# Kernel optimization log

Measured on AMD Instinct MI355X. Metric: run time of the kernel, lower is better.

## Reference

```python
import jax, jax.numpy as jnp
import numpy as np

N_BLOCKS, N_LAYERS = 3, 10
DILATIONS = [2 ** l for _ in range(N_BLOCKS) for l in range(N_LAYERS)] + [1]


def dilate(x, new, old):
    """nsynth-style batch-folding dilation: [n,c,l] -> [n*new/old, c, l*old/new]."""
    if new == old:
        return x
    n, c, l = x.shape
    n_new = n * new // old
    l_new = l * old // new
    # (n,c,l) -> (c,l,n) -> (c,l_new,n_new) -> (n_new,c,l_new)
    return jnp.transpose(jnp.transpose(x, (1, 2, 0)).reshape(c, l_new, n_new), (2, 0, 1))


def conv1d(x, w, b=None, pad=0):
    y = jax.lax.conv_general_dilated(
        x, w, window_strides=(1,), padding=[(pad, pad)],
        dimension_numbers=("NCH", "OIH", "NCH"))
    if b is not None:
        y = y + b[None, :, None]
    return y


def setup_inputs() -> dict:
    key = jax.random.key(0)
    ks = jax.random.split(key, 13)
    s = 0.05
    R, S, Cin, Cout, K, L = 256, 256, 1, 256, 3, 4096
    nl = N_BLOCKS * N_LAYERS
    return {
        "x": jax.random.normal(ks[0], (2, Cin, L), jnp.float32),
        "init_w": jax.random.normal(ks[1], (R, Cin, K), jnp.float32) * s,
        "init_b": jax.random.normal(ks[2], (R,), jnp.float32) * s,
        "iskip_w": jax.random.normal(ks[3], (S, R, 1), jnp.float32) * s,
        "iskip_b": jax.random.normal(ks[4], (S,), jnp.float32) * s,
        "gate_w": jax.random.normal(ks[5], (nl, R, R, K), jnp.float32) * s,
        "gate_b": jax.random.normal(ks[6], (nl, R), jnp.float32) * s,
        "feat_w": jax.random.normal(ks[7], (nl, R, R, K), jnp.float32) * s,
        "feat_b": jax.random.normal(ks[8], (nl, R), jnp.float32) * s,
        "skip_w": jax.random.normal(ks[9], (nl, S, R, 1), jnp.float32) * s,
        "thru_w": jax.random.normal(ks[10], (nl, R, R, 1), jnp.float32) * s,
        "final_w": jax.random.normal(ks[11], (Cout, S, 1), jnp.float32) * s,
        "final_b": jax.random.normal(ks[12], (Cout,), jnp.float32) * s,
    }


def reference(x, init_w, init_b, iskip_w, iskip_b, gate_w, gate_b,
              feat_w, feat_b, skip_w, thru_w, final_w, final_b):
    pad = (init_w.shape[-1] - 1) // 2  # kernel_size=3 -> pad=1
    h = conv1d(x, init_w, init_b, pad=pad)          # [n, R, L]
    s = conv1d(h, iskip_w, iskip_b)                 # [n, S, L]
    for k in range(N_BLOCKS * N_LAYERS):
        d_new, d_old = DILATIONS[k], DILATIONS[k - 1]
        hd = dilate(h, d_new, d_old)                # [n*d, R, L/d]
        g = conv1d(hd, gate_w[k], gate_b[k], pad=pad)
        f = conv1d(hd, feat_w[k], feat_b[k], pad=pad)
        res = jax.nn.sigmoid(g) * jnp.tanh(f)
        h = hd + conv1d(res, thru_w[k])
        s = s + dilate(conv1d(res, skip_w[k]), 1, d_new)
    return conv1d(s, final_w, final_b)
```

## Files before the change

kernel.cpp:

```cpp
#include <hip/hip_runtime.h>


#define TS 8192
#define NL 30
#define NBLK 256

typedef __attribute__((ext_vector_type(8))) short bf16x8;
typedef __attribute__((ext_vector_type(4))) float f32x4;

__device__ __forceinline__ unsigned short f2bf(float f) {
    union { float f; unsigned int u; } v; v.f = f;
    unsigned int u = v.u;
    u += 0x7fffu + ((u >> 16) & 1u);
    return (unsigned short)(u >> 16);
}

__device__ __forceinline__ void gload_lds16(const void* g, void* l) {
    __builtin_amdgcn_global_load_lds(
        (const __attribute__((address_space(1))) void*)g,
        (__attribute__((address_space(3))) void*)l, 16, 0, 0);
}

#define VMW8()  asm volatile("s_waitcnt vmcnt(8)" ::: "memory")
#define VMW4()  asm volatile("s_waitcnt vmcnt(4)" ::: "memory")
#define VMW0()  asm volatile("s_waitcnt vmcnt(0)" ::: "memory")
#define LGKM0() asm volatile("s_waitcnt lgkmcnt(0)" ::: "memory")
#define SBAR()  __builtin_amdgcn_s_barrier()
#define MFMA16(a, b, c) __builtin_amdgcn_mfma_f32_16x16x32_bf16((a), (b), (c), 0, 0, 0)

__device__ __forceinline__ int swz_jb(int bid) {
    return ((bid & 7) << 5) | (bid >> 3);
}

__global__ void prep_weights_kernel(
    const float* __restrict__ gw, const float* __restrict__ fw,
    const float* __restrict__ tw, const float* __restrict__ sw,
    const float* __restrict__ iw, const float* __restrict__ fnw,
    unsigned short* __restrict__ Wgf, unsigned short* __restrict__ Wts,
    unsigned short* __restrict__ Wib, unsigned short* __restrict__ Wfb)
{
    const int idx = blockIdx.x * blockDim.x + threadIdx.x;
    const int stride = gridDim.x * blockDim.x;
    const int n_gf = NL * 3 * 512 * 256;
    for (int i = idx; i < n_gf; i += stride) {
        int ci = i & 255;
        int o  = (i >> 8) & 511;
        int r  = i >> 17;
        int t  = r % 3;
        int k  = r / 3;
        float v = (o < 256) ? gw[((k * 256 + o) * 256 + ci) * 3 + t]
                            : fw[((k * 256 + (o - 256)) * 256 + ci) * 3 + t];
        Wgf[i] = f2bf(v);
    }
    const int n_ts = NL * 512 * 256;
    for (int i = idx; i < n_ts; i += stride) {
        int ci = i & 255;
        int o  = (i >> 8) & 511;
        int k  = i >> 17;
        float v = (o < 256) ? tw[(k * 256 + o) * 256 + ci]
                            : sw[(k * 256 + (o - 256)) * 256 + ci];
        Wts[i] = f2bf(v);
    }
    for (int i = idx; i < 256 * 256; i += stride) Wib[i] = f2bf(iw[i]);
    for (int i = idx; i < 256 * 256; i += stride) Wfb[i] = f2bf(fnw[i]);
}

__device__ __forceinline__ void grid_barrier(unsigned* cnt, unsigned target, int tid) {
    __syncthreads();
    if (tid == 0) {
        __hip_atomic_fetch_add(cnt, 1u, __ATOMIC_RELEASE, __HIP_MEMORY_SCOPE_AGENT);
        while (__hip_atomic_load(cnt, __ATOMIC_RELAXED, __HIP_MEMORY_SCOPE_AGENT) < target)
            __builtin_amdgcn_s_sleep(2);
        (void)__hip_atomic_load(cnt, __ATOMIC_ACQUIRE, __HIP_MEMORY_SCOPE_AGENT);
    }
    __syncthreads();
}

__device__ __forceinline__ void stage_chunk(
    const unsigned short* __restrict__ Wgf_k,
    const unsigned short* __restrict__ Wts_k,
    unsigned short* B_lds, int c, int w, int lane)
{
    const int buf  = c % 3;
    const int rsub = lane >> 2;
    const int slot = (lane & 3) ^ ((lane >> 3) & 3);
    unsigned short* dst = B_lds + w * 6144 + buf * 2048;
    if (c < 24) {
        const int t = c >> 3, kc = c & 7;
        const unsigned short* Wb = Wgf_k + (t * 512 + 32 * w) * 256 + kc * 32 + slot * 8;
        #pragma unroll
        for (int q = 0; q < 4; ++q) {
            const int r_loc = q * 16 + rsub;
            const int grow  = (q < 2) ? r_loc : (224 + r_loc);
            gload_lds16(Wb + grow * 256, dst + q * 512);
        }
    } else {
        const int kc = c - 24;
        const unsigned short* Wb = Wts_k + (64 * w) * 256 + kc * 32 + slot * 8;
        #pragma unroll
        for (int q = 0; q < 4; ++q)
            gload_lds16(Wb + (q * 16 + rsub) * 256, dst + q * 512);
    }
}

__device__ __forceinline__ bf16x8 bread(const unsigned short* Bw, int r, int krow)
{
    const int slot = krow ^ ((r >> 1) & 3);
    return *(const bf16x8*)(Bw + r * 32 + slot * 8);
}

__global__ __launch_bounds__(512, 2)
void wavenet_kernel(const float* __restrict__ x,
                    const float* __restrict__ init_w,
                    const float* __restrict__ init_b,
                    const unsigned short* __restrict__ Wib,
                    const float* __restrict__ ib,
                    const unsigned short* __restrict__ Wgf,
                    const unsigned short* __restrict__ Wts,
                    const float* __restrict__ gbA,
                    const float* __restrict__ fbA,
                    const unsigned short* __restrict__ Wfb,
                    const float* __restrict__ fbias,
                    unsigned short* __restrict__ Hb0,
                    unsigned short* __restrict__ Hb1,
                    float* __restrict__ out,
                    unsigned* __restrict__ counter)
{
    __shared__ __align__(16) unsigned short A_lds[3 * 32 * 256];
    __shared__ __align__(16) unsigned short B_lds[8 * 3 * 2048];

    const int tid  = threadIdx.x;
    const int lane = tid & 63;
    const int w    = tid >> 6;
    const int j0   = swz_jb(blockIdx.x) * 32;
    const int arow = lane & 15;
    const int krow = lane >> 4;
    const int aswz = (arow & 7) << 4;
    const int cg0  = w * 32;
    const int c0   = w * 64;
    const int cs0  = (w - 4) * 64;

    f32x4 state[2][4];

    if (w < 4) {
        #pragma unroll
        for (int rt = 0; rt < 2; ++rt)
            #pragma unroll
            for (int fc = 0; fc < 4; ++fc) {
                #pragma unroll
                for (int i = 0; i < 4; ++i) {
                    const int row = rt * 16 + krow * 4 + i;
                    const int col = c0 + fc * 16 + arow;
                    const int j   = j0 + row;
                    float acc = init_b[col];
                    #pragma unroll
                    for (int t = 0; t < 3; ++t) {
                        const int i2 = j + 2 * t - 2;
                        if (i2 >= 0 && i2 < TS)
                            acc += init_w[col * 3 + t] * x[(i2 & 1) * 4096 + (i2 >> 1)];
                    }
                    state[rt][fc][i] = acc;
                    const unsigned short hb = f2bf(acc);
                    Hb0[(j << 8) + col] = hb;
                    A_lds[((32 + row) << 8) + (((col << 1) ^ ((row & 7) << 4)) >> 1)] = hb;
                }
            }
    }
    LGKM0(); SBAR();

    if (w >= 4) {
        #pragma unroll
        for (int rt = 0; rt < 2; ++rt)
            #pragma unroll
            for (int fc = 0; fc < 4; ++fc) {
                const float b = ib[cs0 + fc * 16 + arow];
                state[rt][fc] = (f32x4){b, b, b, b};
            }
        #pragma unroll
        for (int kc = 0; kc < 8; ++kc) {
            const int aoff = ((kc * 64 + krow * 16) ^ aswz) >> 1;
            const bf16x8 a0 = *(const bf16x8*)(A_lds + ((32 + arow) << 8) + aoff);
            const bf16x8 a1 = *(const bf16x8*)(A_lds + ((48 + arow) << 8) + aoff);
            const int koff = kc * 32 + krow * 8;
            #pragma unroll
            for (int fc = 0; fc < 4; ++fc) {
                const bf16x8 bb = *(const bf16x8*)(Wib + ((cs0 + fc * 16 + arow) << 8) + koff);
                state[0][fc] = MFMA16(a0, bb, state[0][fc]);
                state[1][fc] = MFMA16(a1, bb, state[1][fc]);
            }
        }
    }

    stage_chunk(Wgf, Wts, B_lds, 0, w, lane);
    stage_chunk(Wgf, Wts, B_lds, 1, w, lane);

    unsigned target = NBLK;
    grid_barrier(counter, target, tid);

    const unsigned short* Hb_in = Hb0;
    unsigned short*       Hb_out = Hb1;

    for (int k = 0; k < NL; ++k) {
        const int d = 2 << (k % 10);
        const unsigned short* Wgf_k = Wgf + (size_t)k * 3 * 512 * 256;
        const unsigned short* Wts_k = Wts + (size_t)k * 512 * 256;
        const float gv0 = gbA[k * 256 + cg0 + arow];
        const float gv1 = gbA[k * 256 + cg0 + 16 + arow];
        const float fv0 = fbA[k * 256 + cg0 + arow];
        const float fv1 = fbA[k * 256 + cg0 + 16 + arow];

        #pragma unroll
        for (int q = 0; q < 4; ++q) {
            const int cc  = tid + q * 512;
            const int c16 = cc & 31;
            const int m   = (cc >> 5) & 31;
            const int t   = (cc >> 10) << 1;
            const int r   = j0 + m + (t - 1) * d;
            uint4 v = make_uint4(0u, 0u, 0u, 0u);
            if (r >= 0 && r < TS)
                v = *(const uint4*)(Hb_in + (r << 8) + (c16 << 3));
            const int sb = (c16 << 4) ^ ((m & 7) << 4);
            *(uint4*)(A_lds + ((t * 32 + m) << 8) + (sb >> 1)) = v;
        }
        LGKM0(); SBAR();

        f32x4 accG[2][2], accF[2][2];
        accG[0][0] = (f32x4){gv0, gv0, gv0, gv0};
        accG[1][0] = accG[0][0];
        accG[0][1] = (f32x4){gv1, gv1, gv1, gv1};
        accG[1][1] = accG[0][1];
        accF[0][0] = (f32x4){fv0, fv0, fv0, fv0};
        accF[1][0] = accF[0][0];
        accF[0][1] = (f32x4){fv1, fv1, fv1, fv1};
        accF[1][1] = accF[0][1];

        #pragma unroll
        for (int c = 0; c < 24; ++c) {
            stage_chunk(Wgf_k, Wts_k, B_lds, c + 2, w, lane);
            VMW8();
            const int t = c >> 3, kc = c & 7;
            const int aoff = ((kc * 64 + krow * 16) ^ aswz) >> 1;
            const unsigned short* At = A_lds + ((t * 32 + arow) << 8);
            const bf16x8 a0 = *(const bf16x8*)(At + aoff);
            const bf16x8 a1 = *(const bf16x8*)(At + (16 << 8) + aoff);
            const unsigned short* Bw = B_lds + w * 6144 + (c % 3) * 2048;
            const bf16x8 bg0 = bread(Bw, arow, krow);
            const bf16x8 bg1 = bread(Bw, 16 + arow, krow);
            const bf16x8 bf0 = bread(Bw, 32 + arow, krow);
            const bf16x8 bf1 = bread(Bw, 48 + arow, krow);
            accG[0][0] = MFMA16(a0, bg0, accG[0][0]);
            accG[1][0] = MFMA16(a1, bg0, accG[1][0]);
            accG[0][1] = MFMA16(a0, bg1, accG[0][1]);
            accG[1][1] = MFMA16(a1, bg1, accG[1][1]);
            accF[0][0] = MFMA16(a0, bf0, accF[0][0]);
            accF[1][0] = MFMA16(a1, bf0, accF[1][0]);
            accF[0][1] = MFMA16(a0, bf1, accF[0][1]);
            accF[1][1] = MFMA16(a1, bf1, accF[1][1]);
        }

        LGKM0(); SBAR();

        #pragma unroll
        for (int rt = 0; rt < 2; ++rt)
            #pragma unroll
            for (int fc = 0; fc < 2; ++fc)
                #pragma unroll
                for (int i = 0; i < 4; ++i) {
                    const float g = accG[rt][fc][i];
                    const float f = accF[rt][fc][i];
                    const float sg = 1.0f / (1.0f + __expf(-g));
                    const float e2 = __expf(2.0f * f);
                    const float th = 1.0f - 2.0f / (e2 + 1.0f);
                    const float rr = sg * th;
                    const int row = rt * 16 + krow * 4 + i;
                    const int col = cg0 + fc * 16 + arow;
                    A_lds[(row << 8) + (((col << 1) ^ ((row & 7) << 4)) >> 1)] = f2bf(rr);
                }
        LGKM0(); SBAR();

        f32x4 acc2[2][4];
        #pragma unroll
        for (int rt = 0; rt < 2; ++rt)
            #pragma unroll
            for (int fc = 0; fc < 4; ++fc)
                acc2[rt][fc] = state[rt][fc];

        #pragma unroll
        for (int p = 0; p < 8; ++p) {
            if (p < 6) { stage_chunk(Wgf_k, Wts_k, B_lds, 26 + p, w, lane); VMW8(); }
            else if (p == 6) { VMW4(); }
            else { VMW0(); }
            const int aoff = ((p * 64 + krow * 16) ^ aswz) >> 1;
            const bf16x8 a0 = *(const bf16x8*)(A_lds + (arow << 8) + aoff);
            const bf16x8 a1 = *(const bf16x8*)(A_lds + ((16 + arow) << 8) + aoff);
            const unsigned short* Bw = B_lds + w * 6144 + ((24 + p) % 3) * 2048;
            const bf16x8 b0 = bread(Bw, arow, krow);
            const bf16x8 b1 = bread(Bw, 16 + arow, krow);
            const bf16x8 b2 = bread(Bw, 32 + arow, krow);
            const bf16x8 b3 = bread(Bw, 48 + arow, krow);
            acc2[0][0] = MFMA16(a0, b0, acc2[0][0]);
            acc2[1][0] = MFMA16(a1, b0, acc2[1][0]);
            acc2[0][1] = MFMA16(a0, b1, acc2[0][1]);
            acc2[1][1] = MFMA16(a1, b1, acc2[1][1]);
            acc2[0][2] = MFMA16(a0, b2, acc2[0][2]);
            acc2[1][2] = MFMA16(a1, b2, acc2[1][2]);
            acc2[0][3] = MFMA16(a0, b3, acc2[0][3]);
            acc2[1][3] = MFMA16(a1, b3, acc2[1][3]);
        }

        #pragma unroll
        for (int rt = 0; rt < 2; ++rt)
            #pragma unroll
            for (int fc = 0; fc < 4; ++fc)
                state[rt][fc] = acc2[rt][fc];

        if (k < NL - 1) {
            if (w < 4) {
                #pragma unroll
                for (int rt = 0; rt < 2; ++rt)
                    #pragma unroll
                    for (int fc = 0; fc < 4; ++fc)
                        #pragma unroll
                        for (int i = 0; i < 4; ++i) {
                            const int row = rt * 16 + krow * 4 + i;
                            const int col = c0 + fc * 16 + arow;
                            const unsigned short hb = f2bf(state[rt][fc][i]);
                            Hb_out[((j0 + row) << 8) + col] = hb;
                            A_lds[((32 + row) << 8) + (((col << 1) ^ ((row & 7) << 4)) >> 1)] = hb;
                        }
            }
            stage_chunk(Wgf_k + 3 * 512 * 256, Wts_k + 512 * 256, B_lds, 0, w, lane);
            stage_chunk(Wgf_k + 3 * 512 * 256, Wts_k + 512 * 256, B_lds, 1, w, lane);

            target += NBLK;
            grid_barrier(counter, target, tid);

            unsigned short* tmp = (unsigned short*)Hb_in;
            Hb_in = Hb_out; Hb_out = tmp;
        } else {
            SBAR();
            if (w >= 4) {
                #pragma unroll
                for (int rt = 0; rt < 2; ++rt)
                    #pragma unroll
                    for (int fc = 0; fc < 4; ++fc)
                        #pragma unroll
                        for (int i = 0; i < 4; ++i) {
                            const int row = rt * 16 + krow * 4 + i;
                            const int col = cs0 + fc * 16 + arow;
                            A_lds[(row << 8) + (((col << 1) ^ ((row & 7) << 4)) >> 1)] =
                                f2bf(state[rt][fc][i]);
                        }
            }
            LGKM0(); SBAR();
        }
    }

    {
        const int m0 = w * 32;
        f32x4 facc[2][2];
        #pragma unroll
        for (int rt = 0; rt < 2; ++rt)
            #pragma unroll
            for (int fc = 0; fc < 2; ++fc)
                facc[rt][fc] = (f32x4){0.f, 0.f, 0.f, 0.f};

        #pragma unroll
        for (int kc = 0; kc < 8; ++kc) {
            const int koff = kc * 32 + krow * 8;
            const bf16x8 a0 = *(const bf16x8*)(Wfb + ((m0 + arow) << 8) + koff);
            const bf16x8 a1 = *(const bf16x8*)(Wfb + ((m0 + 16 + arow) << 8) + koff);
            const int aoff = ((kc * 64 + krow * 16) ^ aswz) >> 1;
            const bf16x8 b0 = *(const bf16x8*)(A_lds + (arow << 8) + aoff);
            const bf16x8 b1 = *(const bf16x8*)(A_lds + ((16 + arow) << 8) + aoff);
            facc[0][0] = MFMA16(a0, b0, facc[0][0]);
            facc[1][0] = MFMA16(a1, b0, facc[1][0]);
            facc[0][1] = MFMA16(a0, b1, facc[0][1]);
            facc[1][1] = MFMA16(a1, b1, facc[1][1]);
        }

        #pragma unroll
        for (int rt = 0; rt < 2; ++rt)
            #pragma unroll
            for (int fc = 0; fc < 2; ++fc)
                #pragma unroll
                for (int i = 0; i < 4; ++i) {
                    const int co = m0 + rt * 16 + krow * 4 + i;
                    const int jj = j0 + fc * 16 + arow;
                    out[((jj & 1) << 20) + (co << 12) + (jj >> 1)] = facc[rt][fc][i] + fbias[co];
                }
    }
}

extern "C" void kernel_launch(void* const* d_in, const int* in_sizes, int n_in,
                              void* d_out, int out_size, void* d_ws, size_t ws_size,
                              hipStream_t stream)
{
    const float* x       = (const float*)d_in[0];
    const float* init_w  = (const float*)d_in[1];
    const float* init_b  = (const float*)d_in[2];
    const float* iskip_w = (const float*)d_in[3];
    const float* iskip_b = (const float*)d_in[4];
    const float* gate_w  = (const float*)d_in[5];
    const float* gate_b  = (const float*)d_in[6];
    const float* feat_w  = (const float*)d_in[7];
    const float* feat_b  = (const float*)d_in[8];
    const float* skip_w  = (const float*)d_in[9];
    const float* thru_w  = (const float*)d_in[10];
    const float* final_w = (const float*)d_in[11];
    const float* final_b = (const float*)d_in[12];

    char* ws = (char*)d_ws;
    size_t off = 0;
    auto alloc = [&](size_t bytes) {
        void* p = ws + off;
        off += (bytes + 255) & ~(size_t)255;
        return p;
    };
    unsigned short* Wgf = (unsigned short*)alloc((size_t)NL * 3 * 512 * 256 * 2);
    unsigned short* Wts = (unsigned short*)alloc((size_t)NL * 512 * 256 * 2);
    unsigned short* Wib = (unsigned short*)alloc(256 * 256 * 2);
    unsigned short* Wfb = (unsigned short*)alloc(256 * 256 * 2);
    unsigned short* Hb0 = (unsigned short*)alloc((size_t)TS * 256 * 2);
    unsigned short* Hb1 = (unsigned short*)alloc((size_t)TS * 256 * 2);
    unsigned*       cnt = (unsigned*)alloc(256);

    hipMemsetAsync((void*)cnt, 0, 256, stream);
    prep_weights_kernel<<<2048, 256, 0, stream>>>(gate_w, feat_w, thru_w, skip_w,
                                                  iskip_w, final_w, Wgf, Wts, Wib, Wfb);
    wavenet_kernel<<<NBLK, 512, 0, stream>>>(
        x, init_w, init_b, Wib, iskip_b, Wgf, Wts, gate_b, feat_b,
        Wfb, final_b, Hb0, Hb1, (float*)d_out, cnt);
}
```

Baseline: 909.7 us.

## Pre-swizzle weights into MFMA fragment order and stream them into a register ring

The prep kernel now writes each layer's gate/feature and through/skip weights as one array already arranged in per-wave, per-lane MFMA B-fragment order. The main kernel loads these fragments from global memory straight into a 4-deep register ring, prefetching three chunks ahead and across layer boundaries. This drops the LDS weight staging buffer, the global-to-LDS loads, the swizzled LDS reads and the vmcnt waits. In exchange it uses more vector registers, which may affect occupancy under the 512x2 launch bounds, and it depends on the compiler placing the memory waits well.

After: 1.047 ms. +15.1%, slower.

```diff
diff --git a/kernel.cpp b/kernel.cpp
--- a/kernel.cpp
+++ b/kernel.cpp
@@ -4,6 +4,7 @@
 #define TS 8192
 #define NL 30
 #define NBLK 256
+#define LSTRIDE 524288
 
 typedef __attribute__((ext_vector_type(8))) short bf16x8;
 typedef __attribute__((ext_vector_type(4))) float f32x4;
@@ -15,15 +16,6 @@
     return (unsigned short)(u >> 16);
 }
 
-__device__ __forceinline__ void gload_lds16(const void* g, void* l) {
-    __builtin_amdgcn_global_load_lds(
-        (const __attribute__((address_space(1))) void*)g,
-        (__attribute__((address_space(3))) void*)l, 16, 0, 0);
-}
-
-#define VMW8()  asm volatile("s_waitcnt vmcnt(8)" ::: "memory")
-#define VMW4()  asm volatile("s_waitcnt vmcnt(4)" ::: "memory")
-#define VMW0()  asm volatile("s_waitcnt vmcnt(0)" ::: "memory")
 #define LGKM0() asm volatile("s_waitcnt lgkmcnt(0)" ::: "memory")
 #define SBAR()  __builtin_amdgcn_s_barrier()
 #define MFMA16(a, b, c) __builtin_amdgcn_mfma_f32_16x16x32_bf16((a), (b), (c), 0, 0, 0)
@@ -36,30 +28,38 @@
     const float* __restrict__ gw, const float* __restrict__ fw,
     const float* __restrict__ tw, const float* __restrict__ sw,
     const float* __restrict__ iw, const float* __restrict__ fnw,
-    unsigned short* __restrict__ Wgf, unsigned short* __restrict__ Wts,
+    unsigned short* __restrict__ WF,
     unsigned short* __restrict__ Wib, unsigned short* __restrict__ Wfb)
 {
     const int idx = blockIdx.x * blockDim.x + threadIdx.x;
     const int stride = gridDim.x * blockDim.x;
-    const int n_gf = NL * 3 * 512 * 256;
-    for (int i = idx; i < n_gf; i += stride) {
-        int ci = i & 255;
-        int o  = (i >> 8) & 511;
-        int r  = i >> 17;
-        int t  = r % 3;
-        int k  = r / 3;
-        float v = (o < 256) ? gw[((k * 256 + o) * 256 + ci) * 3 + t]
-                            : fw[((k * 256 + (o - 256)) * 256 + ci) * 3 + t];
-        Wgf[i] = f2bf(v);
-    }
-    const int n_ts = NL * 512 * 256;
-    for (int i = idx; i < n_ts; i += stride) {
-        int ci = i & 255;
-        int o  = (i >> 8) & 511;
-        int k  = i >> 17;
-        float v = (o < 256) ? tw[(k * 256 + o) * 256 + ci]
-                            : sw[(k * 256 + (o - 256)) * 256 + ci];
-        Wts[i] = f2bf(v);
+    const int total = NL * 65536;
+    for (int i = idx; i < total; i += stride) {
+        const int L = i & 63;
+        const int q = (i >> 6) & 3;
+        const int w = (i >> 8) & 7;
+        const int c = (i >> 11) & 31;
+        const int k = i >> 16;
+        const int n  = L & 15;
+        const int k8 = (L >> 4) * 8;
+        unsigned short* dst = WF + (size_t)i * 8;
+        if (c < 24) {
+            const int t  = c >> 3;
+            const int kc = c & 7;
+            const int kbase = kc * 32 + k8;
+            const int row = 32 * w + (q & 1) * 16 + n;
+            const float* src = ((q < 2) ? gw : fw) + ((k * 256 + row) * 256 + kbase) * 3 + t;
+            #pragma unroll
+            for (int j = 0; j < 8; ++j) dst[j] = f2bf(src[j * 3]);
+        } else {
+            const int kc = c - 24;
+            const int kbase = kc * 32 + k8;
+            const int col = 64 * w + q * 16 + n;
+            const float* src = ((col < 256) ? (tw + (k * 256 + col) * 256)
+                                            : (sw + (k * 256 + col - 256) * 256)) + kbase;
+            #pragma unroll
+            for (int j = 0; j < 8; ++j) dst[j] = f2bf(src[j]);
+        }
     }
     for (int i = idx; i < 256 * 256; i += stride) Wib[i] = f2bf(iw[i]);
     for (int i = idx; i < 256 * 256; i += stride) Wfb[i] = f2bf(fnw[i]);
@@ -76,47 +76,13 @@
     __syncthreads();
 }
 
-__device__ __forceinline__ void stage_chunk(
-    const unsigned short* __restrict__ Wgf_k,
-    const unsigned short* __restrict__ Wts_k,
-    unsigned short* B_lds, int c, int w, int lane)
-{
-    const int buf  = c % 3;
-    const int rsub = lane >> 2;
-    const int slot = (lane & 3) ^ ((lane >> 3) & 3);
-    unsigned short* dst = B_lds + w * 6144 + buf * 2048;
-    if (c < 24) {
-        const int t = c >> 3, kc = c & 7;
-        const unsigned short* Wb = Wgf_k + (t * 512 + 32 * w) * 256 + kc * 32 + slot * 8;
-        #pragma unroll
-        for (int q = 0; q < 4; ++q) {
-            const int r_loc = q * 16 + rsub;
-            const int grow  = (q < 2) ? r_loc : (224 + r_loc);
-            gload_lds16(Wb + grow * 256, dst + q * 512);
-        }
-    } else {
-        const int kc = c - 24;
-        const unsigned short* Wb = Wts_k + (64 * w) * 256 + kc * 32 + slot * 8;
-        #pragma unroll
-        for (int q = 0; q < 4; ++q)
-            gload_lds16(Wb + (q * 16 + rsub) * 256, dst + q * 512);
-    }
-}
-
-__device__ __forceinline__ bf16x8 bread(const unsigned short* Bw, int r, int krow)
-{
-    const int slot = krow ^ ((r >> 1) & 3);
-    return *(const bf16x8*)(Bw + r * 32 + slot * 8);
-}
-
 __global__ __launch_bounds__(512, 2)
 void wavenet_kernel(const float* __restrict__ x,
                     const float* __restrict__ init_w,
                     const float* __restrict__ init_b,
                     const unsigned short* __restrict__ Wib,
                     const float* __restrict__ ib,
-                    const unsigned short* __restrict__ Wgf,
-                    const unsigned short* __restrict__ Wts,
+                    const unsigned short* __restrict__ WF,
                     const float* __restrict__ gbA,
                     const float* __restrict__ fbA,
                     const unsigned short* __restrict__ Wfb,
@@ -127,7 +93,6 @@
                     unsigned* __restrict__ counter)
 {
     __shared__ __align__(16) unsigned short A_lds[3 * 32 * 256];
-    __shared__ __align__(16) unsigned short B_lds[8 * 3 * 2048];
 
     const int tid  = threadIdx.x;
     const int lane = tid & 63;
@@ -141,6 +106,16 @@
     const int cs0  = (w - 4) * 64;
 
     f32x4 state[2][4];
+    bf16x8 ring[4][4];
+
+    const unsigned short* wb0 = WF + w * 2048 + lane * 8;
+
+#define LOADC(BASE, C, S)                                                      \
+    do {                                                                       \
+        _Pragma("unroll")                                                      \
+        for (int _q = 0; _q < 4; ++_q)                                         \
+            ring[S][_q] = *(const bf16x8*)((BASE) + (C) * 16384 + _q * 512);   \
+    } while (0)
 
     if (w < 4) {
         #pragma unroll
@@ -191,8 +166,9 @@
         }
     }
 
-    stage_chunk(Wgf, Wts, B_lds, 0, w, lane);
-    stage_chunk(Wgf, Wts, B_lds, 1, w, lane);
+    LOADC(wb0, 0, 0);
+    LOADC(wb0, 1, 1);
+    LOADC(wb0, 2, 2);
 
     unsigned target = NBLK;
     grid_barrier(counter, target, tid);
@@ -202,8 +178,8 @@
 
     for (int k = 0; k < NL; ++k) {
         const int d = 2 << (k % 10);
-        const unsigned short* Wgf_k = Wgf + (size_t)k * 3 * 512 * 256;
-        const unsigned short* Wts_k = Wts + (size_t)k * 512 * 256;
+        const unsigned short* wbk = WF + (size_t)k * LSTRIDE + w * 2048 + lane * 8;
+        const unsigned short* wbn = wbk + LSTRIDE;
         const float gv0 = gbA[k * 256 + cg0 + arow];
         const float gv1 = gbA[k * 256 + cg0 + 16 + arow];
         const float fv0 = fbA[k * 256 + cg0 + arow];
@@ -236,26 +212,21 @@
 
         #pragma unroll
         for (int c = 0; c < 24; ++c) {
-            stage_chunk(Wgf_k, Wts_k, B_lds, c + 2, w, lane);
-            VMW8();
+            LOADC(wbk, c + 3, (c + 3) & 3);
             const int t = c >> 3, kc = c & 7;
             const int aoff = ((kc * 64 + krow * 16) ^ aswz) >> 1;
             const unsigned short* At = A_lds + ((t * 32 + arow) << 8);
             const bf16x8 a0 = *(const bf16x8*)(At + aoff);
             const bf16x8 a1 = *(const bf16x8*)(At + (16 << 8) + aoff);
-            const unsigned short* Bw = B_lds + w * 6144 + (c % 3) * 2048;
-            const bf16x8 bg0 = bread(Bw, arow, krow);
-            const bf16x8 bg1 = bread(Bw, 16 + arow, krow);
-            const bf16x8 bf0 = bread(Bw, 32 + arow, krow);
-            const bf16x8 bf1 = bread(Bw, 48 + arow, krow);
-            accG[0][0] = MFMA16(a0, bg0, accG[0][0]);
-            accG[1][0] = MFMA16(a1, bg0, accG[1][0]);
-            accG[0][1] = MFMA16(a0, bg1, accG[0][1]);
-            accG[1][1] = MFMA16(a1, bg1, accG[1][1]);
-            accF[0][0] = MFMA16(a0, bf0, accF[0][0]);
-            accF[1][0] = MFMA16(a1, bf0, accF[1][0]);
-            accF[0][1] = MFMA16(a0, bf1, accF[0][1]);
-            accF[1][1] = MFMA16(a1, bf1, accF[1][1]);
+            const int s = c & 3;
+            accG[0][0] = MFMA16(a0, ring[s][0], accG[0][0]);
+            accG[1][0] = MFMA16(a1, ring[s][0], accG[1][0]);
+            accG[0][1] = MFMA16(a0, ring[s][1], accG[0][1]);
+            accG[1][1] = MFMA16(a1, ring[s][1], accG[1][1]);
+            accF[0][0] = MFMA16(a0, ring[s][2], accF[0][0]);
+            accF[1][0] = MFMA16(a1, ring[s][2], accF[1][0]);
+            accF[0][1] = MFMA16(a0, ring[s][3], accF[0][1]);
+            accF[1][1] = MFMA16(a1, ring[s][3], accF[1][1]);
         }
 
         LGKM0(); SBAR();
@@ -287,25 +258,24 @@
 
         #pragma unroll
         for (int p = 0; p < 8; ++p) {
-            if (p < 6) { stage_chunk(Wgf_k, Wts_k, B_lds, 26 + p, w, lane); VMW8(); }
-            else if (p == 6) { VMW4(); }
-            else { VMW0(); }
+            const int m = 24 + p;
+            if (m + 3 < 32) {
+                LOADC(wbk, m + 3, (m + 3) & 3);
+            } else if (k < NL - 1) {
+                LOADC(wbn, m + 3 - 32, (m + 3) & 3);
+            }
             const int aoff = ((p * 64 + krow * 16) ^ aswz) >> 1;
             const bf16x8 a0 = *(const bf16x8*)(A_lds + (arow << 8) + aoff);
             const bf16x8 a1 = *(const bf16x8*)(A_lds + ((16 + arow) << 8) + aoff);
-            const unsigned short* Bw = B_lds + w * 6144 + ((24 + p) % 3) * 2048;
-            const bf16x8 b0 = bread(Bw, arow, krow);
-            const bf16x8 b1 = bread(Bw, 16 + arow, krow);
-            const bf16x8 b2 = bread(Bw, 32 + arow, krow);
-            const bf16x8 b3 = bread(Bw, 48 + arow, krow);
-            acc2[0][0] = MFMA16(a0, b0, acc2[0][0]);
-            acc2[1][0] = MFMA16(a1, b0, acc2[1][0]);
-            acc2[0][1] = MFMA16(a0, b1, acc2[0][1]);
-            acc2[1][1] = MFMA16(a1, b1, acc2[1][1]);
-            acc2[0][2] = MFMA16(a0, b2, acc2[0][2]);
-            acc2[1][2] = MFMA16(a1, b2, acc2[1][2]);
-            acc2[0][3] = MFMA16(a0, b3, acc2[0][3]);
-            acc2[1][3] = MFMA16(a1, b3, acc2[1][3]);
+            const int s = m & 3;
+            acc2[0][0] = MFMA16(a0, ring[s][0], acc2[0][0]);
+            acc2[1][0] = MFMA16(a1, ring[s][0], acc2[1][0]);
+            acc2[0][1] = MFMA16(a0, ring[s][1], acc2[0][1]);
+            acc2[1][1] = MFMA16(a1, ring[s][1], acc2[1][1]);
+            acc2[0][2] = MFMA16(a0, ring[s][2], acc2[0][2]);
+            acc2[1][2] = MFMA16(a1, ring[s][2], acc2[1][2]);
+            acc2[0][3] = MFMA16(a0, ring[s][3], acc2[0][3]);
+            acc2[1][3] = MFMA16(a1, ring[s][3], acc2[1][3]);
         }
 
         #pragma unroll
@@ -329,16 +299,13 @@
                             A_lds[((32 + row) << 8) + (((col << 1) ^ ((row & 7) << 4)) >> 1)] = hb;
                         }
             }
-            stage_chunk(Wgf_k + 3 * 512 * 256, Wts_k + 512 * 256, B_lds, 0, w, lane);
-            stage_chunk(Wgf_k + 3 * 512 * 256, Wts_k + 512 * 256, B_lds, 1, w, lane);
-
             target += NBLK;
             grid_barrier(counter, target, tid);
 
             unsigned short* tmp = (unsigned short*)Hb_in;
             Hb_in = Hb_out; Hb_out = tmp;
         } else {
-            SBAR();
+            LGKM0(); SBAR();
             if (w >= 4) {
                 #pragma unroll
                 for (int rt = 0; rt < 2; ++rt)
@@ -390,6 +357,7 @@
                     out[((jj & 1) << 20) + (co << 12) + (jj >> 1)] = facc[rt][fc][i] + fbias[co];
                 }
     }
+#undef LOADC
 }
 
 extern "C" void kernel_launch(void* const* d_in, const int* in_sizes, int n_in,
@@ -417,8 +385,7 @@
         off += (bytes + 255) & ~(size_t)255;
         return p;
     };
-    unsigned short* Wgf = (unsigned short*)alloc((size_t)NL * 3 * 512 * 256 * 2);
-    unsigned short* Wts = (unsigned short*)alloc((size_t)NL * 512 * 256 * 2);
+    unsigned short* WF  = (unsigned short*)alloc((size_t)NL * LSTRIDE * 2);
     unsigned short* Wib = (unsigned short*)alloc(256 * 256 * 2);
     unsigned short* Wfb = (unsigned short*)alloc(256 * 256 * 2);
     unsigned short* Hb0 = (unsigned short*)alloc((size_t)TS * 256 * 2);
@@ -427,8 +394,8 @@
 
     hipMemsetAsync((void*)cnt, 0, 256, stream);
     prep_weights_kernel<<<2048, 256, 0, stream>>>(gate_w, feat_w, thru_w, skip_w,
-                                                  iskip_w, final_w, Wgf, Wts, Wib, Wfb);
+                                                  iskip_w, final_w, WF, Wib, Wfb);
     wavenet_kernel<<<NBLK, 512, 0, stream>>>(
-        x, init_w, init_b, Wib, iskip_b, Wgf, Wts, gate_b, feat_b,
+        x, init_w, init_b, Wib, iskip_b, WF, gate_b, feat_b,
         Wfb, final_b, Hb0, Hb1, (float*)d_out, cnt);
 }
```

## Split work across 16 waves per block instead of 8

Applied to the files above, without the earlier changes.

Doubles the block size from 512 to 1024 threads. Each wave now owns half as many output columns, so per-wave accumulators, LDS staging and the pipelined wait counts are all halved and reindexed. This adds latency hiding through more waves per CU within the persistent grid-barrier design. It also moves the prefetch of the next layer's weights ahead of the h writeback, and the smaller per-wave MFMA tiles reduce operand reuse while block barriers must now synchronise more waves.

Measured after the change: 1.227 ms. +34.9%, slower.

```diff
diff --git a/kernel.cpp b/kernel.cpp
--- a/kernel.cpp
+++ b/kernel.cpp
@@ -21,8 +21,8 @@
         (__attribute__((address_space(3))) void*)l, 16, 0, 0);
 }
 
-#define VMW8()  asm volatile("s_waitcnt vmcnt(8)" ::: "memory")
 #define VMW4()  asm volatile("s_waitcnt vmcnt(4)" ::: "memory")
+#define VMW2()  asm volatile("s_waitcnt vmcnt(2)" ::: "memory")
 #define VMW0()  asm volatile("s_waitcnt vmcnt(0)" ::: "memory")
 #define LGKM0() asm volatile("s_waitcnt lgkmcnt(0)" ::: "memory")
 #define SBAR()  __builtin_amdgcn_s_barrier()
@@ -76,40 +76,35 @@
     __syncthreads();
 }
 
-__device__ __forceinline__ void stage_chunk(
+__device__ __forceinline__ void stage16(
     const unsigned short* __restrict__ Wgf_k,
     const unsigned short* __restrict__ Wts_k,
-    unsigned short* B_lds, int c, int w, int lane)
-{
-    const int buf  = c % 3;
+    unsigned short* B_lds, int c, int buf, int v, int lane)
+{
     const int rsub = lane >> 2;
     const int slot = (lane & 3) ^ ((lane >> 3) & 3);
-    unsigned short* dst = B_lds + w * 6144 + buf * 2048;
+    unsigned short* dst = B_lds + v * 3072 + buf * 1024;
     if (c < 24) {
         const int t = c >> 3, kc = c & 7;
-        const unsigned short* Wb = Wgf_k + (t * 512 + 32 * w) * 256 + kc * 32 + slot * 8;
-        #pragma unroll
-        for (int q = 0; q < 4; ++q) {
-            const int r_loc = q * 16 + rsub;
-            const int grow  = (q < 2) ? r_loc : (224 + r_loc);
-            gload_lds16(Wb + grow * 256, dst + q * 512);
-        }
+        const unsigned short* Wb = Wgf_k + kc * 32 + slot * 8;
+        gload_lds16(Wb + ((t * 512 + 16 * v + rsub) << 8), dst);
+        gload_lds16(Wb + ((t * 512 + 256 + 16 * v + rsub) << 8), dst + 512);
     } else {
         const int kc = c - 24;
-        const unsigned short* Wb = Wts_k + (64 * w) * 256 + kc * 32 + slot * 8;
-        #pragma unroll
-        for (int q = 0; q < 4; ++q)
-            gload_lds16(Wb + (q * 16 + rsub) * 256, dst + q * 512);
-    }
-}
-
-__device__ __forceinline__ bf16x8 bread(const unsigned short* Bw, int r, int krow)
-{
-    const int slot = krow ^ ((r >> 1) & 3);
-    return *(const bf16x8*)(Bw + r * 32 + slot * 8);
-}
-
-__global__ __launch_bounds__(512, 2)
+        const unsigned short* Wb = Wts_k + kc * 32 + slot * 8;
+        gload_lds16(Wb + ((32 * v + rsub) << 8), dst);
+        gload_lds16(Wb + ((32 * v + 16 + rsub) << 8), dst + 512);
+    }
+}
+
+__device__ __forceinline__ bf16x8 bread16(const unsigned short* B_lds,
+                                          int v, int buf, int r, int krow)
+{
+    return *(const bf16x8*)(B_lds + v * 3072 + buf * 1024 + r * 32 +
+                            ((krow ^ ((r >> 1) & 3)) << 3));
+}
+
+__global__ __launch_bounds__(1024, 4)
 void wavenet_kernel(const float* __restrict__ x,
                     const float* __restrict__ init_w,
                     const float* __restrict__ init_b,
@@ -127,72 +122,72 @@
                     unsigned* __restrict__ counter)
 {
     __shared__ __align__(16) unsigned short A_lds[3 * 32 * 256];
-    __shared__ __align__(16) unsigned short B_lds[8 * 3 * 2048];
+    __shared__ __align__(16) unsigned short B_lds[16 * 3 * 1024];
 
     const int tid  = threadIdx.x;
     const int lane = tid & 63;
-    const int w    = tid >> 6;
+    const int v    = tid >> 6;
     const int j0   = swz_jb(blockIdx.x) * 32;
     const int arow = lane & 15;
     const int krow = lane >> 4;
     const int aswz = (arow & 7) << 4;
-    const int cg0  = w * 32;
-    const int c0   = w * 64;
-    const int cs0  = (w - 4) * 64;
-
-    f32x4 state[2][4];
-
-    if (w < 4) {
-        #pragma unroll
-        for (int rt = 0; rt < 2; ++rt)
-            #pragma unroll
-            for (int fc = 0; fc < 4; ++fc) {
+
+    f32x4 state[2][2];
+
+    if (v < 8) {
+        const int c0 = v * 32;
+        #pragma unroll
+        for (int ct = 0; ct < 2; ++ct) {
+            const int col = c0 + ct * 16 + arow;
+            const float w0 = init_w[col * 3];
+            const float w1 = init_w[col * 3 + 1];
+            const float w2 = init_w[col * 3 + 2];
+            const float b  = init_b[col];
+            #pragma unroll
+            for (int rt = 0; rt < 2; ++rt)
                 #pragma unroll
                 for (int i = 0; i < 4; ++i) {
                     const int row = rt * 16 + krow * 4 + i;
-                    const int col = c0 + fc * 16 + arow;
-                    const int j   = j0 + row;
-                    float acc = init_b[col];
-                    #pragma unroll
-                    for (int t = 0; t < 3; ++t) {
-                        const int i2 = j + 2 * t - 2;
-                        if (i2 >= 0 && i2 < TS)
-                            acc += init_w[col * 3 + t] * x[(i2 & 1) * 4096 + (i2 >> 1)];
-                    }
-                    state[rt][fc][i] = acc;
+                    const int j = j0 + row;
+                    float acc = b + w1 * x[(j & 1) * 4096 + (j >> 1)];
+                    int i2 = j - 2;
+                    if (i2 >= 0) acc += w0 * x[(i2 & 1) * 4096 + (i2 >> 1)];
+                    i2 = j + 2;
+                    if (i2 < TS) acc += w2 * x[(i2 & 1) * 4096 + (i2 >> 1)];
+                    state[rt][ct][i] = acc;
                     const unsigned short hb = f2bf(acc);
                     Hb0[(j << 8) + col] = hb;
                     A_lds[((32 + row) << 8) + (((col << 1) ^ ((row & 7) << 4)) >> 1)] = hb;
                 }
-            }
+        }
     }
     LGKM0(); SBAR();
 
-    if (w >= 4) {
-        #pragma unroll
-        for (int rt = 0; rt < 2; ++rt)
-            #pragma unroll
-            for (int fc = 0; fc < 4; ++fc) {
-                const float b = ib[cs0 + fc * 16 + arow];
-                state[rt][fc] = (f32x4){b, b, b, b};
-            }
+    if (v >= 8) {
+        const int cs = (v - 8) * 32;
+        #pragma unroll
+        for (int ct = 0; ct < 2; ++ct) {
+            const float b = ib[cs + ct * 16 + arow];
+            state[0][ct] = (f32x4){b, b, b, b};
+            state[1][ct] = state[0][ct];
+        }
         #pragma unroll
         for (int kc = 0; kc < 8; ++kc) {
             const int aoff = ((kc * 64 + krow * 16) ^ aswz) >> 1;
             const bf16x8 a0 = *(const bf16x8*)(A_lds + ((32 + arow) << 8) + aoff);
             const bf16x8 a1 = *(const bf16x8*)(A_lds + ((48 + arow) << 8) + aoff);
             const int koff = kc * 32 + krow * 8;
-            #pragma unroll
-            for (int fc = 0; fc < 4; ++fc) {
-                const bf16x8 bb = *(const bf16x8*)(Wib + ((cs0 + fc * 16 + arow) << 8) + koff);
-                state[0][fc] = MFMA16(a0, bb, state[0][fc]);
-                state[1][fc] = MFMA16(a1, bb, state[1][fc]);
-            }
-        }
-    }
-
-    stage_chunk(Wgf, Wts, B_lds, 0, w, lane);
-    stage_chunk(Wgf, Wts, B_lds, 1, w, lane);
+            const bf16x8 b0 = *(const bf16x8*)(Wib + ((cs + arow) << 8) + koff);
+            const bf16x8 b1 = *(const bf16x8*)(Wib + ((cs + 16 + arow) << 8) + koff);
+            state[0][0] = MFMA16(a0, b0, state[0][0]);
+            state[1][0] = MFMA16(a1, b0, state[1][0]);
+            state[0][1] = MFMA16(a0, b1, state[0][1]);
+            state[1][1] = MFMA16(a1, b1, state[1][1]);
+        }
+    }
+
+    stage16(Wgf, Wts, B_lds, 0, 0, v, lane);
+    stage16(Wgf, Wts, B_lds, 1, 1, v, lane);
 
     unsigned target = NBLK;
     grid_barrier(counter, target, tid);
@@ -202,60 +197,46 @@
 
     for (int k = 0; k < NL; ++k) {
         const int d = 2 << (k % 10);
-        const unsigned short* Wgf_k = Wgf + (size_t)k * 3 * 512 * 256;
-        const unsigned short* Wts_k = Wts + (size_t)k * 512 * 256;
-        const float gv0 = gbA[k * 256 + cg0 + arow];
-        const float gv1 = gbA[k * 256 + cg0 + 16 + arow];
-        const float fv0 = fbA[k * 256 + cg0 + arow];
-        const float fv1 = fbA[k * 256 + cg0 + 16 + arow];
-
-        #pragma unroll
-        for (int q = 0; q < 4; ++q) {
-            const int cc  = tid + q * 512;
+        const unsigned short* Wgf_k = Wgf + (size_t)k * 393216;
+        const unsigned short* Wts_k = Wts + (size_t)k * 131072;
+
+        #pragma unroll
+        for (int q = 0; q < 2; ++q) {
+            const int cc  = tid + q * 1024;
             const int c16 = cc & 31;
             const int m   = (cc >> 5) & 31;
             const int t   = (cc >> 10) << 1;
             const int r   = j0 + m + (t - 1) * d;
-            uint4 v = make_uint4(0u, 0u, 0u, 0u);
+            uint4 val = make_uint4(0u, 0u, 0u, 0u);
             if (r >= 0 && r < TS)
-                v = *(const uint4*)(Hb_in + (r << 8) + (c16 << 3));
-            const int sb = (c16 << 4) ^ ((m & 7) << 4);
-            *(uint4*)(A_lds + ((t * 32 + m) << 8) + (sb >> 1)) = v;
+                val = *(const uint4*)(Hb_in + (r << 8) + (c16 << 3));
+            const int sb = ((c16 << 4) ^ ((m & 7) << 4)) >> 1;
+            *(uint4*)(A_lds + ((t * 32 + m) << 8) + sb) = val;
         }
         LGKM0(); SBAR();
 
-        f32x4 accG[2][2], accF[2][2];
-        accG[0][0] = (f32x4){gv0, gv0, gv0, gv0};
-        accG[1][0] = accG[0][0];
-        accG[0][1] = (f32x4){gv1, gv1, gv1, gv1};
-        accG[1][1] = accG[0][1];
-        accF[0][0] = (f32x4){fv0, fv0, fv0, fv0};
-        accF[1][0] = accF[0][0];
-        accF[0][1] = (f32x4){fv1, fv1, fv1, fv1};
-        accF[1][1] = accF[0][1];
+        const float gv = gbA[k * 256 + v * 16 + arow];
+        const float fv = fbA[k * 256 + v * 16 + arow];
+        f32x4 accG[2], accF[2];
+        accG[0] = (f32x4){gv, gv, gv, gv}; accG[1] = accG[0];
+        accF[0] = (f32x4){fv, fv, fv, fv}; accF[1] = accF[0];
 
         #pragma unroll
         for (int c = 0; c < 24; ++c) {
-            stage_chunk(Wgf_k, Wts_k, B_lds, c + 2, w, lane);
-            VMW8();
+            stage16(Wgf_k, Wts_k, B_lds, c + 2, (c + 2) % 3, v, lane);
+            VMW4();
             const int t = c >> 3, kc = c & 7;
             const int aoff = ((kc * 64 + krow * 16) ^ aswz) >> 1;
             const unsigned short* At = A_lds + ((t * 32 + arow) << 8);
             const bf16x8 a0 = *(const bf16x8*)(At + aoff);
             const bf16x8 a1 = *(const bf16x8*)(At + (16 << 8) + aoff);
-            const unsigned short* Bw = B_lds + w * 6144 + (c % 3) * 2048;
-            const bf16x8 bg0 = bread(Bw, arow, krow);
-            const bf16x8 bg1 = bread(Bw, 16 + arow, krow);
-            const bf16x8 bf0 = bread(Bw, 32 + arow, krow);
-            const bf16x8 bf1 = bread(Bw, 48 + arow, krow);
-            accG[0][0] = MFMA16(a0, bg0, accG[0][0]);
-            accG[1][0] = MFMA16(a1, bg0, accG[1][0]);
-            accG[0][1] = MFMA16(a0, bg1, accG[0][1]);
-            accG[1][1] = MFMA16(a1, bg1, accG[1][1]);
-            accF[0][0] = MFMA16(a0, bf0, accF[0][0]);
-            accF[1][0] = MFMA16(a1, bf0, accF[1][0]);
-            accF[0][1] = MFMA16(a0, bf1, accF[0][1]);
-            accF[1][1] = MFMA16(a1, bf1, accF[1][1]);
+            const int buf = c % 3;
+            const bf16x8 bg  = bread16(B_lds, v, buf, arow, krow);
+            const bf16x8 bf_ = bread16(B_lds, v, buf, 16 + arow, krow);
+            accG[0] = MFMA16(a0, bg,  accG[0]);
+            accG[1] = MFMA16(a1, bg,  accG[1]);
+            accF[0] = MFMA16(a0, bf_, accF[0]);
+            accF[1] = MFMA16(a1, bf_, accF[1]);
         }
 
         LGKM0(); SBAR();
@@ -263,93 +244,85 @@
         #pragma unroll
         for (int rt = 0; rt < 2; ++rt)
             #pragma unroll
-            for (int fc = 0; fc < 2; ++fc)
-                #pragma unroll
-                for (int i = 0; i < 4; ++i) {
-                    const float g = accG[rt][fc][i];
-                    const float f = accF[rt][fc][i];
-                    const float sg = 1.0f / (1.0f + __expf(-g));
-                    const float e2 = __expf(2.0f * f);
-                    const float th = 1.0f - 2.0f / (e2 + 1.0f);
-                    const float rr = sg * th;
-                    const int row = rt * 16 + krow * 4 + i;
-                    const int col = cg0 + fc * 16 + arow;
-                    A_lds[(row << 8) + (((col << 1) ^ ((row & 7) << 4)) >> 1)] = f2bf(rr);
-                }
+            for (int i = 0; i < 4; ++i) {
+                const float g = accG[rt][i];
+                const float f = accF[rt][i];
+                const float sg = 1.0f / (1.0f + __expf(-g));
+                const float e2 = __expf(2.0f * f);
+                const float th = 1.0f - 2.0f / (e2 + 1.0f);
+                const float rr = sg * th;
+                const int row = rt * 16 + krow * 4 + i;
+                const int col = v * 16 + arow;
+                A_lds[(row << 8) + (((col << 1) ^ ((row & 7) << 4)) >> 1)] = f2bf(rr);
+            }
         LGKM0(); SBAR();
 
-        f32x4 acc2[2][4];
+        f32x4 acc2[2][2];
         #pragma unroll
         for (int rt = 0; rt < 2; ++rt)
             #pragma unroll
-            for (int fc = 0; fc < 4; ++fc)
-                acc2[rt][fc] = state[rt][fc];
+            for (int ct = 0; ct < 2; ++ct)
+                acc2[rt][ct] = state[rt][ct];
 
         #pragma unroll
         for (int p = 0; p < 8; ++p) {
-            if (p < 6) { stage_chunk(Wgf_k, Wts_k, B_lds, 26 + p, w, lane); VMW8(); }
-            else if (p == 6) { VMW4(); }
-            else { VMW0(); }
+            if (p < 6)      { stage16(Wgf_k, Wts_k, B_lds, 26 + p, (26 + p) % 3, v, lane); VMW4(); }
+            else if (p == 6){ VMW2(); }
+            else            { VMW0(); }
             const int aoff = ((p * 64 + krow * 16) ^ aswz) >> 1;
             const bf16x8 a0 = *(const bf16x8*)(A_lds + (arow << 8) + aoff);
             const bf16x8 a1 = *(const bf16x8*)(A_lds + ((16 + arow) << 8) + aoff);
-            const unsigned short* Bw = B_lds + w * 6144 + ((24 + p) % 3) * 2048;
-            const bf16x8 b0 = bread(Bw, arow, krow);
-            const bf16x8 b1 = bread(Bw, 16 + arow, krow);
-            const bf16x8 b2 = bread(Bw, 32 + arow, krow);
-            const bf16x8 b3 = bread(Bw, 48 + arow, krow);
+            const int buf = p % 3;
+            const bf16x8 b0 = bread16(B_lds, v, buf, arow, krow);
+            const bf16x8 b1 = bread16(B_lds, v, buf, 16 + arow, krow);
             acc2[0][0] = MFMA16(a0, b0, acc2[0][0]);
             acc2[1][0] = MFMA16(a1, b0, acc2[1][0]);
             acc2[0][1] = MFMA16(a0, b1, acc2[0][1]);
             acc2[1][1] = MFMA16(a1, b1, acc2[1][1]);
-            acc2[0][2] = MFMA16(a0, b2, acc2[0][2]);
-            acc2[1][2] = MFMA16(a1, b2, acc2[1][2]);
-            acc2[0][3] = MFMA16(a0, b3, acc2[0][3]);
-            acc2[1][3] = MFMA16(a1, b3, acc2[1][3]);
         }
 
         #pragma unroll
         for (int rt = 0; rt < 2; ++rt)
             #pragma unroll
-            for (int fc = 0; fc < 4; ++fc)
-                state[rt][fc] = acc2[rt][fc];
+            for (int ct = 0; ct < 2; ++ct)
+                state[rt][ct] = acc2[rt][ct];
 
         if (k < NL - 1) {
-            if (w < 4) {
+            stage16(Wgf_k + 393216, Wts_k + 131072, B_lds, 0, 0, v, lane);
+            stage16(Wgf_k + 393216, Wts_k + 131072, B_lds, 1, 1, v, lane);
+
+            if (v < 8) {
                 #pragma unroll
                 for (int rt = 0; rt < 2; ++rt)
                     #pragma unroll
-                    for (int fc = 0; fc < 4; ++fc)
+                    for (int ct = 0; ct < 2; ++ct)
                         #pragma unroll
                         for (int i = 0; i < 4; ++i) {
                             const int row = rt * 16 + krow * 4 + i;
-                            const int col = c0 + fc * 16 + arow;
-                            const unsigned short hb = f2bf(state[rt][fc][i]);
+                            const int col = v * 32 + ct * 16 + arow;
+                            const unsigned short hb = f2bf(state[rt][ct][i]);
                             Hb_out[((j0 + row) << 8) + col] = hb;
                             A_lds[((32 + row) << 8) + (((col << 1) ^ ((row & 7) << 4)) >> 1)] = hb;
                         }
             }
-            stage_chunk(Wgf_k + 3 * 512 * 256, Wts_k + 512 * 256, B_lds, 0, w, lane);
-            stage_chunk(Wgf_k + 3 * 512 * 256, Wts_k + 512 * 256, B_lds, 1, w, lane);
-
             target += NBLK;
             grid_barrier(counter, target, tid);
 
             unsigned short* tmp = (unsigned short*)Hb_in;
             Hb_in = Hb_out; Hb_out = tmp;
         } else {
-            SBAR();
-            if (w >= 4) {
+            LGKM0(); SBAR();
+            if (v >= 8) {
                 #pragma unroll
                 for (int rt = 0; rt < 2; ++rt)
                     #pragma unroll
-                    for (int fc = 0; fc < 4; ++fc)
+                    for (int ct = 0; ct < 2; ++ct)
                         #pragma unroll
                         for (int i = 0; i < 4; ++i) {
                             const int row = rt * 16 + krow * 4 + i;
-                            const int col = cs0 + fc * 16 + arow;
+                            const int col = (v - 8) * 32 + ct * 16 + arow;
                             A_lds[(row << 8) + (((col << 1) ^ ((row & 7) << 4)) >> 1)] =
-                                f2bf(state[rt][fc][i]);
+                                f2bf(state[rt][ct][i]);
                         }
             }
             LGKM0(); SBAR();
@@ -357,38 +330,30 @@
     }
 
     {
-        const int m0 = w * 32;
-        f32x4 facc[2][2];
-        #pragma unroll
-        for (int rt = 0; rt < 2; ++rt)
-            #pragma unroll
-            for (int fc = 0; fc < 2; ++fc)
-                facc[rt][fc] = (f32x4){0.f, 0.f, 0.f, 0.f};
+        const int m0 = v * 16;
+        f32x4 facc[2];
+        facc[0] = (f32x4){0.f, 0.f, 0.f, 0.f};
+        facc[1] = facc[0];
 
         #pragma unroll
         for (int kc = 0; kc < 8; ++kc) {
             const int koff = kc * 32 + krow * 8;
             const bf16x8 a0 = *(const bf16x8*)(Wfb + ((m0 + arow) << 8) + koff);
-            const bf16x8 a1 = *(const bf16x8*)(Wfb + ((m0 + 16 + arow) << 8) + koff);
             const int aoff = ((kc * 64 + krow * 16) ^ aswz) >> 1;
             const bf16x8 b0 = *(const bf16x8*)(A_lds + (arow << 8) + aoff);
             const bf16x8 b1 = *(const bf16x8*)(A_lds + ((16 + arow) << 8) + aoff);
-            facc[0][0] = MFMA16(a0, b0, facc[0][0]);
-            facc[1][0] = MFMA16(a1, b0, facc[1][0]);
-            facc[0][1] = MFMA16(a0, b1, facc[0][1]);
-            facc[1][1] = MFMA16(a1, b1, facc[1][1]);
-        }
-
-        #pragma unroll
-        for (int rt = 0; rt < 2; ++rt)
-            #pragma unroll
-            for (int fc = 0; fc < 2; ++fc)
-                #pragma unroll
-                for (int i = 0; i < 4; ++i) {
-                    const int co = m0 + rt * 16 + krow * 4 + i;
-                    const int jj = j0 + fc * 16 + arow;
-                    out[((jj & 1) << 20) + (co << 12) + (jj >> 1)] = facc[rt][fc][i] + fbias[co];
-                }
+            facc[0] = MFMA16(a0, b0, facc[0]);
+            facc[1] = MFMA16(a0, b1, facc[1]);
+        }
+
+        #pragma unroll
+        for (int ct = 0; ct < 2; ++ct)
+            #pragma unroll
+            for (int i = 0; i < 4; ++i) {
+                const int co = m0 + krow * 4 + i;
+                const int jj = j0 + ct * 16 + arow;
+                out[((jj & 1) << 20) + (co << 12) + (jj >> 1)] = facc[ct][i] + fbias[co];
+            }
     }
 }
 
@@ -428,7 +393,7 @@
     hipMemsetAsync((void*)cnt, 0, 256, stream);
     prep_weights_kernel<<<2048, 256, 0, stream>>>(gate_w, feat_w, thru_w, skip_w,
                                                   iskip_w, final_w, Wgf, Wts, Wib, Wfb);
-    wavenet_kernel<<<NBLK, 512, 0, stream>>>(
+    wavenet_kernel<<<NBLK, 1024, 0, stream>>>(
         x, init_w, init_b, Wib, iskip_b, Wgf, Wts, gate_b, feat_b,
         Wfb, final_b, Hb0, Hb1, (float*)d_out, cnt);
 }
```
